# Kernel optimization log

Measured on AMD Instinct MI355X. Metric: run time of the kernel, lower is better.

The kernel has to match this reference:

```python
import jax, jax.numpy as jnp
import numpy as np

H = 4          # num_heads
K_HOP = 2
EPS = 1e-5


def _ln(x, g, b):
    m = jnp.mean(x, axis=-1, keepdims=True)
    v = jnp.mean((x - m) ** 2, axis=-1, keepdims=True)
    return (x - m) * jax.lax.rsqrt(v + EPS) * g + b


def setup_inputs() -> dict:
    key = jax.random.key(0)
    B, T, N, D = 16, 24, 512, 64
    F = 256
    ks = jax.random.split(key, 16)
    s = 0.02
    inp = {
        'x': jax.random.normal(ks[0], (B, T, N, D), dtype=jnp.float32),
        'adj': jax.random.uniform(ks[1], (N, N), dtype=jnp.float32),
        'Wq': jax.random.normal(ks[2], (D, D), dtype=jnp.float32) * s,
        'bq': jnp.zeros((D,), jnp.float32),
        'Wk': jax.random.normal(ks[3], (D, D), dtype=jnp.float32) * s,
        'bk': jnp.zeros((D,), jnp.float32),
        'Wv': jax.random.normal(ks[4], (D, D), dtype=jnp.float32) * s,
        'bv': jnp.zeros((D,), jnp.float32),
        'Wo': jax.random.normal(ks[5], (D, D), dtype=jnp.float32) * s,
        'bo': jnp.zeros((D,), jnp.float32),
        'gcW': jax.random.normal(ks[6], (K_HOP + 1, D, D), dtype=jnp.float32) * s,
        'gcb': jnp.zeros((K_HOP + 1, D), jnp.float32),
        'W1': jax.random.normal(ks[7], (D, F), dtype=jnp.float32) * s,
        'b1': jnp.zeros((F,), jnp.float32),
        'W2': jax.random.normal(ks[8], (F, D), dtype=jnp.float32) * s,
        'b2': jnp.zeros((D,), jnp.float32),
        'g_t': jnp.ones((D,), jnp.float32), 'b_t': jnp.zeros((D,), jnp.float32),
        'g_g': jnp.ones((D,), jnp.float32), 'b_g': jnp.zeros((D,), jnp.float32),
        'g_f': jnp.ones((D,), jnp.float32), 'b_f': jnp.zeros((D,), jnp.float32),
    }
    return inp


def _forward(x, adj, Wq, bq, Wk, bk, Wv, bv, Wo, bo, gcW, gcb,
             W1, b1, W2, b2, g_t, b_t, g_g, b_g, g_f, b_f):
    B, T, N, D = x.shape
    hd = D // H
    scale = hd ** -0.5

    # ---- temporal multi-head attention (per node, along T) ----
    def heads(y):
        return y.reshape(B, T, N, H, hd)
    q = heads(x @ Wq + bq)
    k = heads(x @ Wk + bk)
    v = heads(x @ Wv + bv)
    scores = jnp.einsum('bqnhd,bknhd->bnhqk', q, k) * scale  # [B,N,H,T,T]
    attn = jax.nn.softmax(scores, axis=-1)
    att = jnp.einsum('bnhqk,bknhd->bqnhd', attn, v).reshape(B, T, N, D)
    att = att @ Wo + bo
    h = _ln(x + att, g_t, b_t)

    # ---- K-hop graph convolution: sum_k A_hat^k X W_k ----
    A = adj + jnp.eye(N, dtype=adj.dtype)
    deg = A.sum(-1)
    dinv = jnp.clip(deg, 1e-12, None) ** -0.5
    Ahat = dinv[:, None] * A * dinv[None, :]  # [N,N], shared across B*T
    prop = h
    gout = prop @ gcW[0] + gcb[0]
    for kk in range(1, K_HOP + 1):
        prop = jnp.einsum('mn,btnd->btmd', Ahat, prop)
        gout = gout + prop @ gcW[kk] + gcb[kk]
    h = _ln(h + gout, g_g, b_g)

    # ---- FFN (exact GELU, as torch default) ----
    f = jax.nn.gelu(h @ W1 + b1, approximate=False) @ W2 + b2
    return _ln(h + f, g_f, b_f)


def reference(x, adj, Wq, bq, Wk, bk, Wv, bv, Wo, bo, gcW, gcb,
              W1, b1, W2, b2, g_t, b_t, g_g, b_g, g_f, b_f):
    return _forward(x, adj, Wq, bq, Wk, bk, Wv, bv, Wo, bo, gcW, gcb,
                    W1, b1, W2, b2, g_t, b_t, g_g, b_g, g_f, b_f)
```

## Files before the change

### kernel.cpp

```cpp
#include <hip/hip_runtime.h>
#include <hip/hip_bf16.h>
#include <math.h>

typedef __hip_bfloat16 bf16;
typedef unsigned short ushort_t;

__device__ __forceinline__ float us2f(ushort_t u){
  union { unsigned u; float f; } v; v.u = ((unsigned)u) << 16; return v.f;
}
__device__ __forceinline__ ushort_t f2us(float f){
  union { __bf16 b; ushort_t u; } v; v.b = (__bf16)f; return v.u;
}

__device__ __forceinline__ float gelu_f(float x){
  float y = x * fmaf(0.0356774081f, x*x, 0.7978845608f);
  float e = __expf(-2.0f*y);
  return x * __builtin_amdgcn_rcpf(1.0f + e);
}

#define B_ 16
#define T_ 24
#define N_ 512
#define D_ 64
#define F_ 256

typedef __attribute__((ext_vector_type(8)))  short  frag8;
typedef __attribute__((ext_vector_type(16))) float  accv16;

__device__ __forceinline__ float wave_sum(float v){
#pragma unroll
  for (int off = 32; off > 0; off >>= 1) v += __shfl_xor(v, off, 64);
  return v;
}

__global__ __launch_bounds__(64) void k_dinv(const float* __restrict__ adj,
                                             float* __restrict__ dinv){
  int m = blockIdx.x;
  float s = 0.f;
  for (int n = threadIdx.x; n < N_; n += 64) s += adj[m*N_ + n];
  s = wave_sum(s);
  if (threadIdx.x == 0){
    float deg = s + 1.0f;
    dinv[m] = rsqrtf(fmaxf(deg, 1e-12f));
  }
}

__global__ __launch_bounds__(256) void k_ahat(const float* __restrict__ adj,
                                              const float* __restrict__ dinv,
                                              ushort_t* __restrict__ AhatB,
                                              ushort_t* __restrict__ AhatBT){
  int idx = blockIdx.x*256 + threadIdx.x;
  int m = idx >> 9, n = idx & (N_-1);
  float a = adj[idx] + (m == n ? 1.f : 0.f);
  ushort_t v = f2us(dinv[m]*a*dinv[n]);
  AhatB[idx] = v;
  AhatBT[n*N_ + m] = v;
}

__global__ __launch_bounds__(256, 4) void k_ah2(
    const ushort_t* __restrict__ A1,
    const ushort_t* __restrict__ A1T,
    ushort_t* __restrict__ A2)
{
  __shared__ __align__(16) ushort_t Ab[64][72];
  __shared__ __align__(16) ushort_t Bb[64][72];
  __shared__ __align__(16) ushort_t Yt[64][72];
  int tid  = threadIdx.x;
  int lane = tid & 63, w = tid >> 6;
  int mw = (w >> 1) * 32, nw = (w & 1) * 32;
  int l31 = lane & 31, lh = lane >> 5;
  int m0 = blockIdx.x * 64, n0 = blockIdx.y * 64;
  int ar = tid >> 3, ac8 = (tid & 7) * 8;

  accv16 acc = {};
  for (int k0 = 0; k0 < N_; k0 += 64){
#pragma unroll
    for (int g = 0; g < 2; g++){
      int rr = ar + g*32;
      *(uint4*)&Ab[rr][ac8] = *(const uint4*)&A1 [(size_t)(m0 + rr)*N_ + k0 + ac8];
      *(uint4*)&Bb[rr][ac8] = *(const uint4*)&A1T[(size_t)(n0 + rr)*N_ + k0 + ac8];
    }
    __syncthreads();
#pragma unroll
    for (int kk = 0; kk < 64; kk += 16){
      frag8 af = *(const frag8*)&Ab[mw + l31][kk + lh*8];
      frag8 bf = *(const frag8*)&Bb[nw + l31][kk + lh*8];
      acc = __builtin_amdgcn_mfma_f32_32x32x16_bf16(af, bf, acc, 0, 0, 0);
    }
    __syncthreads();
  }
#pragma unroll
  for (int r = 0; r < 16; r++){
    int row = mw + (r & 3) + 8*(r >> 2) + 4*lh;
    Yt[row][nw + l31] = f2us(acc[r]);
  }
  __syncthreads();
#pragma unroll
  for (int g = 0; g < 2; g++){
    int rr = ar + g*32;
    *(uint4*)&A2[(size_t)(m0 + rr)*N_ + n0 + ac8] = *(const uint4*)&Yt[rr][ac8];
  }
}

__global__ __launch_bounds__(256) void k_wprep(
    const float* __restrict__ W1, const float* __restrict__ W2,
    const float* __restrict__ Wq, const float* __restrict__ Wk,
    const float* __restrict__ Wv, const float* __restrict__ Wo,
    const float* __restrict__ gcW,
    ushort_t* __restrict__ W1t, ushort_t* __restrict__ W2t,
    ushort_t* __restrict__ Wqt, ushort_t* __restrict__ Wkt,
    ushort_t* __restrict__ Wvt, ushort_t* __restrict__ Wot,
    ushort_t* __restrict__ gWt){
  int o = blockIdx.x*256 + threadIdx.x;
  int f = o >> 6, e = o & 63;
  W1t[o] = f2us(W1[e*256 + f]);
  int d = o >> 8, e2 = o & 255;
  W2t[o] = f2us(W2[e2*64 + d]);
  if (o < 4096){
    int dd = o >> 6, ee = o & 63;
    Wqt[o] = f2us(Wq[ee*64 + dd]);
    Wkt[o] = f2us(Wk[ee*64 + dd]);
    Wvt[o] = f2us(Wv[ee*64 + dd]);
    Wot[o] = f2us(Wo[ee*64 + dd]);
    gWt[o]        = f2us(gcW[       ee*64 + dd]);
    gWt[4096 + o] = f2us(gcW[4096 + ee*64 + dd]);
    gWt[8192 + o] = f2us(gcW[8192 + ee*64 + dd]);
  }
}

__global__ __launch_bounds__(256, 4) void k_attn_m(
    const float* __restrict__ x,
    const ushort_t* __restrict__ Wqt, const float* __restrict__ bq,
    const ushort_t* __restrict__ Wkt, const float* __restrict__ bk,
    const ushort_t* __restrict__ Wvt, const float* __restrict__ bv,
    const ushort_t* __restrict__ Wot, const float* __restrict__ bo,
    const float* __restrict__ g_t, const float* __restrict__ b_t,
    float* __restrict__ h1)
{
  __shared__ __align__(16) char smem[28928];
  ushort_t (*xsA)[72] = (ushort_t(*)[72]) smem;
  ushort_t (*qs)[72]  = (ushort_t(*)[72])(smem + 6912);
  ushort_t (*ks)[72]  = (ushort_t(*)[72])(smem + 13824);
  float    (*Os)[68]  = (float(*)[68])   (smem + 6912);
  ushort_t *vsT       = (ushort_t*)(smem + 20736);

  int tid = threadIdx.x;
  int lane = tid & 63, w = tid >> 6;
  int l31 = lane & 31, lh = lane >> 5;
  int mt = (w >> 1) * 32, nt = (w & 1) * 32;
  int b = blockIdx.x >> 8;
  int n0 = (blockIdx.x & 255) * 2;

  {
    uint4 z4 = {0,0,0,0};
#pragma unroll
    for (int i = 0; i < 2; i++)
      *(uint4*)(smem + 20736 + (tid + i*256)*16) = z4;
  }
#pragma unroll
  for (int i = 0; i < 3; i++){
    int idx = tid + i*256;
    int row = idx >> 4, d4 = (idx & 15) * 4;
    int node = row >= 24;
    int t = row - node*24;
    const float4 v = *(const float4*)&x[(((size_t)b*T_ + t)*N_ + n0 + node)*D_ + d4];
    ushort_t tmp[4] = { f2us(v.x), f2us(v.y), f2us(v.z), f2us(v.w) };
    *(unsigned long long*)&xsA[row][d4] = *(unsigned long long*)tmp;
  }
  __syncthreads();

#pragma unroll
  for (int pj = 0; pj < 3; pj++){
    const ushort_t* Wp = (pj==0 ? Wqt : pj==1 ? Wkt : Wvt);
    accv16 a = {};
#pragma unroll
    for (int kk = 0; kk < 64; kk += 16){
      frag8 af = *(const frag8*)&xsA[mt + l31][kk + lh*8];
      frag8 bf = *(const frag8*)&Wp[(size_t)(nt + l31)*64 + kk + lh*8];
      a = __builtin_amdgcn_mfma_f32_32x32x16_bf16(af, bf, a, 0, 0, 0);
    }
    float bias = (pj==0 ? bq : pj==1 ? bk : bv)[nt + l31];
    if (pj < 2){
      ushort_t (*dst)[72] = (pj==0 ? qs : ks);
#pragma unroll
      for (int r = 0; r < 16; r++){
        int row = mt + (r & 3) + 8*(r >> 2) + 4*lh;
        if (row < 48) dst[row][nt + l31] = f2us(a[r] + bias);
      }
    } else {
      int cl = nt + l31;
#pragma unroll
      for (int r = 0; r < 16; r++){
        int row = mt + (r & 3) + 8*(r >> 2) + 4*lh;
        if (row < 48){
          int node = (row >= 24);
          int t2 = row - node*24;
          int Rr = node*64 + cl;
          vsT[Rr*32 + (((t2 >> 3) ^ ((Rr >> 1) & 3)) << 3) + (t2 & 7)] = f2us(a[r] + bias);
        }
      }
    }
  }
  __syncthreads();

  int vs_s = (l31 >> 1) & 3;
#pragma unroll
  for (int gi = 0; gi < 2; gi++){
    int g = w*2 + gi;
    int node = g >> 2, hh = g & 3;
    accv16 s = {};
    frag8 kf = *(const frag8*)&ks[node*24 + l31][hh*16 + lh*8];
    frag8 qf = *(const frag8*)&qs[node*24 + l31][hh*16 + lh*8];
    s = __builtin_amdgcn_mfma_f32_32x32x16_bf16(kf, qf, s, 0, 0, 0);
    float e[12]; float sm = 0.f;
#pragma unroll
    for (int r = 0; r < 12; r++){ e[r] = __expf(s[r]*0.25f); sm += e[r]; }
    sm += __shfl_xor(sm, 32, 64);
    float rinv = 1.0f / sm;
    union { unsigned long long q; ushort_t u[4]; } a0, a1, a2;
#pragma unroll
    for (int j = 0; j < 4; j++){
      a0.u[j] = f2us(e[j]   * rinv);
      a1.u[j] = f2us(e[4+j] * rinv);
      a2.u[j] = f2us(e[8+j] * rinv);
    }
    unsigned long long send1 = lh ? a0.q : a1.q;
    unsigned long long r1 = __shfl_xor(send1, 32, 64);
    unsigned long long r2 = __shfl_xor(a2.q, 32, 64);
    union { frag8 f; unsigned long long q[2]; } f0, f1;
    f0.q[0] = lh ? r1   : a0.q;
    f0.q[1] = lh ? a1.q : r1;
    f1.q[0] = lh ? 0ULL : a2.q;
    f1.q[1] = lh ? 0ULL : r2;
    int vrow = node*64 + hh*16 + (l31 & 15);
    const ushort_t* vb = &vsT[vrow*32];
    frag8 bf0 = *(const frag8*)&vb[((0 + lh) ^ vs_s) << 3];
    frag8 bf1 = *(const frag8*)&vb[((2 + lh) ^ vs_s) << 3];
    accv16 acc = {};
    acc = __builtin_amdgcn_mfma_f32_32x32x16_bf16(f0.f, bf0, acc, 0, 0, 0);
    acc = __builtin_amdgcn_mfma_f32_32x32x16_bf16(f1.f, bf1, acc, 0, 0, 0);
    if (l31 < 16){
#pragma unroll
      for (int r = 0; r < 12; r++){
        int row = (r & 3) + 8*(r >> 2) + 4*lh;
        xsA[node*24 + row][hh*16 + l31] = f2us(acc[r]);
      }
    }
  }
  __syncthreads();

  accv16 ao = {};
#pragma unroll
  for (int kk = 0; kk < 64; kk += 16){
    frag8 af = *(const frag8*)&xsA[mt + l31][kk + lh*8];
    frag8 bf = *(const frag8*)&Wot[(size_t)(nt + l31)*64 + kk + lh*8];
    ao = __builtin_amdgcn_mfma_f32_32x32x16_bf16(af, bf, ao, 0, 0, 0);
  }
  {
    float bov = bo[nt + l31];
#pragma unroll
    for (int r = 0; r < 16; r++){
      int row = mt + (r & 3) + 8*(r >> 2) + 4*lh;
      if (row < 48) Os[row][nt + l31] = ao[r] + bov;
    }
  }
  __syncthreads();

  {
    int rrow = tid >> 2, seg = (tid & 3) * 16;
    if (rrow < 48){
      int node = rrow >= 24;
      int t = rrow - node*24;
      size_t gbase = (((size_t)b*T_ + t)*N_ + n0 + node)*D_;
      float vb[16]; float s1 = 0.f;
#pragma unroll
      for (int j4 = 0; j4 < 4; j4++){
        float4 xo = *(const float4*)&x[gbase + seg + j4*4];
        float4 ov = *(const float4*)&Os[rrow][seg + j4*4];
        vb[j4*4+0] = ov.x + xo.x;
        vb[j4*4+1] = ov.y + xo.y;
        vb[j4*4+2] = ov.z + xo.z;
        vb[j4*4+3] = ov.w + xo.w;
        s1 += vb[j4*4+0] + vb[j4*4+1] + vb[j4*4+2] + vb[j4*4+3];
      }
      s1 += __shfl_xor(s1, 1, 64); s1 += __shfl_xor(s1, 2, 64);
      float m = s1 * (1.f/64.f);
      float s2 = 0.f;
#pragma unroll
      for (int j = 0; j < 16; j++){ vb[j] -= m; s2 += vb[j]*vb[j]; }
      s2 += __shfl_xor(s2, 1, 64); s2 += __shfl_xor(s2, 2, 64);
      float rstd = rsqrtf(s2 * (1.f/64.f) + 1e-5f);
#pragma unroll
      for (int j4 = 0; j4 < 4; j4++){
        float4 gv = *(const float4*)&g_t[seg + j4*4];
        float4 bv = *(const float4*)&b_t[seg + j4*4];
        float4 st;
        st.x = vb[j4*4+0]*rstd*gv.x + bv.x;
        st.y = vb[j4*4+1]*rstd*gv.y + bv.y;
        st.z = vb[j4*4+2]*rstd*gv.z + bv.z;
        st.w = vb[j4*4+3]*rstd*gv.w + bv.w;
        *(float4*)&h1[gbase + seg + j4*4] = st;
      }
    }
  }
}

__global__ __launch_bounds__(256, 8) void k_hT(const float* __restrict__ h,
                                               ushort_t* __restrict__ hT){
  __shared__ __align__(16) ushort_t tb[64][76];
  int tid = threadIdx.x;
  int n0 = (blockIdx.x & 7) * 64;
  size_t bt = blockIdx.x >> 3;
  const float* src = h + (bt*N_ + n0)*D_;
#pragma unroll
  for (int i = 0; i < 4; i++){
    int q = tid + i*256;
    int row = q >> 4, d4 = (q & 15)*4;
    float4 v = *(const float4*)&src[(size_t)q*4];
    ushort_t tmp[4] = { f2us(v.x), f2us(v.y), f2us(v.z), f2us(v.w) };
    *(unsigned long long*)&tb[row][d4] = *(unsigned long long*)tmp;
  }
  __syncthreads();
  int d = tid >> 2, nseg = (tid & 3)*16;
  ushort_t tmp[16];
#pragma unroll
  for (int j = 0; j < 16; j++){
    int jj = (j + ((d & 7) << 1)) & 15;
    tmp[jj] = tb[nseg + jj][d];
  }
  ushort_t* dst = hT + (bt*D_ + d)*N_ + n0 + nseg;
  *(uint4*)&dst[0] = *(uint4*)&tmp[0];
  *(uint4*)&dst[8] = *(uint4*)&tmp[8];
}

__global__ __launch_bounds__(256, 4) void k_gcffn(
    const ushort_t* __restrict__ A1,
    const ushort_t* __restrict__ A2,
    const ushort_t* __restrict__ XT,
    const ushort_t* __restrict__ gWt,
    const float* __restrict__ gcb,
    const float* __restrict__ g_g, const float* __restrict__ b_g,
    const ushort_t* __restrict__ W1t, const ushort_t* __restrict__ W2t,
    const float* __restrict__ b1, const float* __restrict__ b2,
    const float* __restrict__ g_f, const float* __restrict__ b_f,
    float* __restrict__ h)
{
  __shared__ __align__(16) char smem[27648];
  ushort_t (*R0)[72]  = (ushort_t(*)[72]) smem;
  ushort_t (*R1)[72]  = (ushort_t(*)[72])(smem +  9216);
  ushort_t (*hsA)[72] = (ushort_t(*)[72])(smem + 18432);
  float    (*Sf)[68]  = (float(*)[68])    smem;
  ushort_t (*Uc)[136] = (ushort_t(*)[136])smem;
  float    (*Os)[68]  = (float(*)[68])    smem;

  int tid = threadIdx.x;
  int lane = tid & 63, w = tid >> 6;
  int l31 = lane & 31, lh = lane >> 5;
  int mw = (w >> 1) * 32, nw = (w & 1) * 32;
  int bid = blockIdx.x;
  int m0 = ((bid >> 3) & 7) * 64;
  size_t bt = (size_t)((bid >> 6) * 8 + (bid & 7));
  const ushort_t* Xg = XT + bt * (N_ * D_);
  size_t tokbase = bt * N_ + m0;
  int ar = tid >> 3, ac8 = (tid & 7) * 8;

  accv16 acc1 = {}, acc2 = {};
  for (int k0 = 0; k0 < N_; k0 += 64){
#pragma unroll
    for (int g = 0; g < 2; g++){
      int rr = ar + g*32;
      *(uint4*)&R0 [rr][ac8] = *(const uint4*)&A1[(size_t)(m0 + rr)*N_ + k0 + ac8];
      *(uint4*)&R1 [rr][ac8] = *(const uint4*)&A2[(size_t)(m0 + rr)*N_ + k0 + ac8];
      *(uint4*)&hsA[rr][ac8] = *(const uint4*)&Xg[(size_t)rr*N_ + k0 + ac8];
    }
    __syncthreads();
#pragma unroll
    for (int kk = 0; kk < 64; kk += 16){
      frag8 bf  = *(const frag8*)&hsA[nw + l31][kk + lh*8];
      frag8 af1 = *(const frag8*)&R0 [mw + l31][kk + lh*8];
      frag8 af2 = *(const frag8*)&R1 [mw + l31][kk + lh*8];
      acc1 = __builtin_amdgcn_mfma_f32_32x32x16_bf16(af1, bf, acc1, 0, 0, 0);
      acc2 = __builtin_amdgcn_mfma_f32_32x32x16_bf16(af2, bf, acc2, 0, 0, 0);
    }
    __syncthreads();
  }

#pragma unroll
  for (int r = 0; r < 16; r++){
    int row = mw + (r & 3) + 8*(r >> 2) + 4*lh;
    R1[row][nw + l31] = f2us(acc1[r]);
    R0[row][nw + l31] = f2us(acc2[r]);
  }
#pragma unroll
  for (int i = 0; i < 4; i++){
    int q = tid + i*256;
    int row = q >> 4, d4 = (q & 15) * 4;
    float4 v = *(const float4*)&h[tokbase*64 + (size_t)q*4];
    ushort_t tmp[4] = { f2us(v.x), f2us(v.y), f2us(v.z), f2us(v.w) };
    *(unsigned long long*)&hsA[row][d4] = *(unsigned long long*)tmp;
  }
  __syncthreads();

  accv16 ag = {};
#pragma unroll
  for (int kk = 0; kk < 64; kk += 16){
    frag8 a0f = *(const frag8*)&hsA[mw + l31][kk + lh*8];
    frag8 b0f = *(const frag8*)&gWt[(size_t)(nw + l31)*64 + kk + lh*8];
    ag = __builtin_amdgcn_mfma_f32_32x32x16_bf16(a0f, b0f, ag, 0, 0, 0);
  }
#pragma unroll
  for (int kk = 0; kk < 64; kk += 16){
    frag8 a1f = *(const frag8*)&R1[mw + l31][kk + lh*8];
    frag8 b1f = *(const frag8*)&gWt[4096 + (size_t)(nw + l31)*64 + kk + lh*8];
    ag = __builtin_amdgcn_mfma_f32_32x32x16_bf16(a1f, b1f, ag, 0, 0, 0);
  }
#pragma unroll
  for (int kk = 0; kk < 64; kk += 16){
    frag8 a2f = *(const frag8*)&R0[mw + l31][kk + lh*8];
    frag8 b2f = *(const frag8*)&gWt[8192 + (size_t)(nw + l31)*64 + kk + lh*8];
    ag = __builtin_amdgcn_mfma_f32_32x32x16_bf16(a2f, b2f, ag, 0, 0, 0);
  }
  __syncthreads();

  {
    int col = nw + l31;
    float bs = gcb[col] + gcb[64 + col] + gcb[128 + col];
#pragma unroll
    for (int r = 0; r < 16; r++){
      int row = mw + (r & 3) + 8*(r >> 2) + 4*lh;
      Sf[row][col] = ag[r] + h[(tokbase + row)*64 + col] + bs;
    }
  }
  __syncthreads();

  int rrow = tid >> 2, seg = (tid & 3) * 16;
  float h2r[16];
  {
    float vb[16]; float s1 = 0.f;
#pragma unroll
    for (int j4 = 0; j4 < 4; j4++){
      float4 v = *(const float4*)&Sf[rrow][seg + j4*4];
      vb[j4*4+0] = v.x; vb[j4*4+1] = v.y; vb[j4*4+2] = v.z; vb[j4*4+3] = v.w;
      s1 += v.x + v.y + v.z + v.w;
    }
    s1 += __shfl_xor(s1, 1, 64); s1 += __shfl_xor(s1, 2, 64);
    float m = s1 * (1.f/64.f);
    float s2 = 0.f;
#pragma unroll
    for (int j = 0; j < 16; j++){ vb[j] -= m; s2 += vb[j]*vb[j]; }
    s2 += __shfl_xor(s2, 1, 64); s2 += __shfl_xor(s2, 2, 64);
    float rstd = rsqrtf(s2 * (1.f/64.f) + 1e-5f);
    ushort_t tmp[16];
#pragma unroll
    for (int j4 = 0; j4 < 4; j4++){
      float4 gv = *(const float4*)&g_g[seg + j4*4];
      float4 bv = *(const float4*)&b_g[seg + j4*4];
      h2r[j4*4+0] = vb[j4*4+0]*rstd*gv.x + bv.x;
      h2r[j4*4+1] = vb[j4*4+1]*rstd*gv.y + bv.y;
      h2r[j4*4+2] = vb[j4*4+2]*rstd*gv.z + bv.z;
      h2r[j4*4+3] = vb[j4*4+3]*rstd*gv.w + bv.w;
    }
#pragma unroll
    for (int j = 0; j < 16; j++) tmp[j] = f2us(h2r[j]);
    *(uint4*)&hsA[rrow][seg]     = *(uint4*)&tmp[0];
    *(uint4*)&hsA[rrow][seg + 8] = *(uint4*)&tmp[8];
  }
  __syncthreads();

  int mw1 = (w & 1) * 32, nA = (w >> 1) * 32;
  int mw2 = (w >> 1) * 32, dw = (w & 1) * 32;
  accv16 accO = {};
#pragma unroll
  for (int f0 = 0; f0 < F_; f0 += 128){
    if (f0) __syncthreads();
    accv16 accA = {}, accB = {};
#pragma unroll
    for (int kk = 0; kk < 64; kk += 16){
      frag8 af  = *(const frag8*)&hsA[mw1 + l31][kk + lh*8];
      frag8 b0  = *(const frag8*)&W1t[(size_t)(f0 + nA + l31)*64 + kk + lh*8];
      frag8 b1f = *(const frag8*)&W1t[(size_t)(f0 + nA + 64 + l31)*64 + kk + lh*8];
      accA = __builtin_amdgcn_mfma_f32_32x32x16_bf16(af, b0,  accA, 0, 0, 0);
      accB = __builtin_amdgcn_mfma_f32_32x32x16_bf16(af, b1f, accB, 0, 0, 0);
    }
    {
      float bA = b1[f0 + nA + l31];
      float bB = b1[f0 + nA + 64 + l31];
#pragma unroll
      for (int r = 0; r < 16; r++){
        int row = mw1 + (r & 3) + 8*(r >> 2) + 4*lh;
        Uc[row][nA + l31]      = f2us(gelu_f(accA[r] + bA));
        Uc[row][nA + 64 + l31] = f2us(gelu_f(accB[r] + bB));
      }
    }
    __syncthreads();
#pragma unroll
    for (int kk = 0; kk < 128; kk += 16){
      frag8 af = *(const frag8*)&Uc[mw2 + l31][kk + lh*8];
      frag8 bf = *(const frag8*)&W2t[(size_t)(dw + l31)*256 + f0 + kk + lh*8];
      accO = __builtin_amdgcn_mfma_f32_32x32x16_bf16(af, bf, accO, 0, 0, 0);
    }
  }
  __syncthreads();
  {
    float b2v = b2[dw + l31];
#pragma unroll
    for (int r = 0; r < 16; r++){
      int row = mw2 + (r & 3) + 8*(r >> 2) + 4*lh;
      Os[row][dw + l31] = accO[r] + b2v;
    }
  }
  __syncthreads();

  {
    float vb[16]; float s1 = 0.f;
#pragma unroll
    for (int j4 = 0; j4 < 4; j4++){
      float4 v = *(const float4*)&Os[rrow][seg + j4*4];
      vb[j4*4+0] = v.x + h2r[j4*4+0];
      vb[j4*4+1] = v.y + h2r[j4*4+1];
      vb[j4*4+2] = v.z + h2r[j4*4+2];
      vb[j4*4+3] = v.w + h2r[j4*4+3];
      s1 += vb[j4*4+0] + vb[j4*4+1] + vb[j4*4+2] + vb[j4*4+3];
    }
    s1 += __shfl_xor(s1, 1, 64); s1 += __shfl_xor(s1, 2, 64);
    float m = s1 * (1.f/64.f);
    float s2 = 0.f;
#pragma unroll
    for (int j = 0; j < 16; j++){ vb[j] -= m; s2 += vb[j]*vb[j]; }
    s2 += __shfl_xor(s2, 1, 64); s2 += __shfl_xor(s2, 2, 64);
    float rstd = rsqrtf(s2 * (1.f/64.f) + 1e-5f);
#pragma unroll
    for (int j4 = 0; j4 < 4; j4++){
      float4 gv = *(const float4*)&g_f[seg + j4*4];
      float4 bv = *(const float4*)&b_f[seg + j4*4];
      float4 st;
      st.x = vb[j4*4+0]*rstd*gv.x + bv.x;
      st.y = vb[j4*4+1]*rstd*gv.y + bv.y;
      st.z = vb[j4*4+2]*rstd*gv.z + bv.z;
      st.w = vb[j4*4+3]*rstd*gv.w + bv.w;
      *(float4*)&h[(tokbase + rrow)*64 + seg + j4*4] = st;
    }
  }
}

extern "C" void kernel_launch(void* const* d_in, const int* in_sizes, int n_in,
                              void* d_out, int out_size, void* d_ws, size_t ws_size,
                              hipStream_t stream)
{
  const float* x   = (const float*)d_in[0];
  const float* adj = (const float*)d_in[1];
  const float* Wq  = (const float*)d_in[2];
  const float* bq  = (const float*)d_in[3];
  const float* Wk  = (const float*)d_in[4];
  const float* bk  = (const float*)d_in[5];
  const float* Wv  = (const float*)d_in[6];
  const float* bv  = (const float*)d_in[7];
  const float* Wo  = (const float*)d_in[8];
  const float* bo  = (const float*)d_in[9];
  const float* gcW = (const float*)d_in[10];
  const float* gcb = (const float*)d_in[11];
  const float* W1  = (const float*)d_in[12];
  const float* b1  = (const float*)d_in[13];
  const float* W2  = (const float*)d_in[14];
  const float* b2  = (const float*)d_in[15];
  const float* g_t = (const float*)d_in[16];
  const float* b_t = (const float*)d_in[17];
  const float* g_g = (const float*)d_in[18];
  const float* b_g = (const float*)d_in[19];
  const float* g_f = (const float*)d_in[20];
  const float* b_f = (const float*)d_in[21];

  const size_t MD = (size_t)B_*T_*N_*D_;
  const size_t NN = (size_t)N_*N_;
  float* dinv = (float*)d_ws;
  ushort_t* AhatB  = (ushort_t*)(dinv + 512);
  ushort_t* AhatBT = AhatB + NN;
  ushort_t* AhatB2 = AhatBT + NN;
  ushort_t* hT  = AhatB2 + NN;
  ushort_t* W1t = hT + MD;
  ushort_t* W2t = W1t + 256*64;
  ushort_t* Wqt = W2t + 64*256;
  ushort_t* Wkt = Wqt + 4096;
  ushort_t* Wvt = Wkt + 4096;
  ushort_t* Wot = Wvt + 4096;
  ushort_t* gWt = Wot + 4096;
  float* h = (float*)d_out;

  k_dinv<<<N_, 64, 0, stream>>>(adj, dinv);
  k_ahat<<<(N_*N_)/256, 256, 0, stream>>>(adj, dinv, AhatB, AhatBT);
  k_wprep<<<64, 256, 0, stream>>>(W1, W2, Wq, Wk, Wv, Wo, gcW,
                                  W1t, W2t, Wqt, Wkt, Wvt, Wot, gWt);
  k_ah2<<<dim3(8, 8), 256, 0, stream>>>(AhatB, AhatBT, AhatB2);
  k_attn_m<<<B_*N_/2, 256, 0, stream>>>(x, Wqt,bq, Wkt,bk, Wvt,bv, Wot,bo, g_t,b_t, h);
  k_hT<<<B_*T_*8, 256, 0, stream>>>(h, hT);
  k_gcffn<<<(N_/64) * B_ * T_, 256, 0, stream>>>(AhatB, AhatB2, hT, gWt,
                                                 gcb, g_g, b_g,
                                                 W1t, W2t, b1, b2, g_f, b_f, h);
}
```

Before: 340.8 us.

## Process two bt slices per block in graph-conv kernel to reuse Ahat tiles

Each k_gcffn block now handles two (b,t) slices sharing the same 64-row Ahat/Ahat² tiles, so each A tile loaded into shared memory feeds four MFMA accumulators instead of two. The grid is halved and shared memory grows to 36 KB. The epilogue (graph-conv weight GEMMs, layernorm, FFN) runs sequentially for each slice. The change cuts global and L2 traffic for Ahat, at the cost of more registers (four accumulators plus two h2r arrays), which may lower occupancy under the launch_bounds(256,4) hint.

```diff
diff --git a/kernel.cpp b/kernel.cpp
--- a/kernel.cpp
+++ b/kernel.cpp
@@ -345,10 +345,11 @@
     const float* __restrict__ g_f, const float* __restrict__ b_f,
     float* __restrict__ h)
 {
-  __shared__ __align__(16) char smem[27648];
-  ushort_t (*R0)[72]  = (ushort_t(*)[72]) smem;
-  ushort_t (*R1)[72]  = (ushort_t(*)[72])(smem +  9216);
-  ushort_t (*hsA)[72] = (ushort_t(*)[72])(smem + 18432);
+  __shared__ __align__(16) char smem[36864];
+  ushort_t (*RA1)[72] = (ushort_t(*)[72]) smem;
+  ushort_t (*RA2)[72] = (ushort_t(*)[72])(smem +  9216);
+  ushort_t (*RX0)[72] = (ushort_t(*)[72])(smem + 18432);
+  ushort_t (*RX1)[72] = (ushort_t(*)[72])(smem + 27648);
   float    (*Sf)[68]  = (float(*)[68])    smem;
   ushort_t (*Uc)[136] = (ushort_t(*)[136])smem;
   float    (*Os)[68]  = (float(*)[68])    smem;
@@ -358,189 +359,244 @@
   int l31 = lane & 31, lh = lane >> 5;
   int mw = (w >> 1) * 32, nw = (w & 1) * 32;
   int bid = blockIdx.x;
+  int xq = bid & 7;
   int m0 = ((bid >> 3) & 7) * 64;
-  size_t bt = (size_t)((bid >> 6) * 8 + (bid & 7));
-  const ushort_t* Xg = XT + bt * (N_ * D_);
-  size_t tokbase = bt * N_ + m0;
+  int q  = bid >> 6;
+  size_t bt0 = (size_t)(q*16 + xq);
+  size_t bt1 = bt0 + 8;
+  const ushort_t* Xg0 = XT + bt0 * (N_ * D_);
+  const ushort_t* Xg1 = XT + bt1 * (N_ * D_);
+  size_t tokb0 = bt0 * N_ + m0;
+  size_t tokb1 = bt1 * N_ + m0;
   int ar = tid >> 3, ac8 = (tid & 7) * 8;
 
-  accv16 acc1 = {}, acc2 = {};
+  accv16 a1s0 = {}, a2s0 = {}, a1s1 = {}, a2s1 = {};
   for (int k0 = 0; k0 < N_; k0 += 64){
 #pragma unroll
     for (int g = 0; g < 2; g++){
       int rr = ar + g*32;
-      *(uint4*)&R0 [rr][ac8] = *(const uint4*)&A1[(size_t)(m0 + rr)*N_ + k0 + ac8];
-      *(uint4*)&R1 [rr][ac8] = *(const uint4*)&A2[(size_t)(m0 + rr)*N_ + k0 + ac8];
-      *(uint4*)&hsA[rr][ac8] = *(const uint4*)&Xg[(size_t)rr*N_ + k0 + ac8];
-    }
-    __syncthreads();
-#pragma unroll
-    for (int kk = 0; kk < 64; kk += 16){
-      frag8 bf  = *(const frag8*)&hsA[nw + l31][kk + lh*8];
-      frag8 af1 = *(const frag8*)&R0 [mw + l31][kk + lh*8];
-      frag8 af2 = *(const frag8*)&R1 [mw + l31][kk + lh*8];
-      acc1 = __builtin_amdgcn_mfma_f32_32x32x16_bf16(af1, bf, acc1, 0, 0, 0);
-      acc2 = __builtin_amdgcn_mfma_f32_32x32x16_bf16(af2, bf, acc2, 0, 0, 0);
-    }
-    __syncthreads();
-  }
-
-#pragma unroll
-  for (int r = 0; r < 16; r++){
-    int row = mw + (r & 3) + 8*(r >> 2) + 4*lh;
-    R1[row][nw + l31] = f2us(acc1[r]);
-    R0[row][nw + l31] = f2us(acc2[r]);
-  }
-#pragma unroll
-  for (int i = 0; i < 4; i++){
-    int q = tid + i*256;
-    int row = q >> 4, d4 = (q & 15) * 4;
-    float4 v = *(const float4*)&h[tokbase*64 + (size_t)q*4];
-    ushort_t tmp[4] = { f2us(v.x), f2us(v.y), f2us(v.z), f2us(v.w) };
-    *(unsigned long long*)&hsA[row][d4] = *(unsigned long long*)tmp;
-  }
-  __syncthreads();
-
-  accv16 ag = {};
-#pragma unroll
-  for (int kk = 0; kk < 64; kk += 16){
-    frag8 a0f = *(const frag8*)&hsA[mw + l31][kk + lh*8];
-    frag8 b0f = *(const frag8*)&gWt[(size_t)(nw + l31)*64 + kk + lh*8];
-    ag = __builtin_amdgcn_mfma_f32_32x32x16_bf16(a0f, b0f, ag, 0, 0, 0);
-  }
-#pragma unroll
-  for (int kk = 0; kk < 64; kk += 16){
-    frag8 a1f = *(const frag8*)&R1[mw + l31][kk + lh*8];
-    frag8 b1f = *(const frag8*)&gWt[4096 + (size_t)(nw + l31)*64 + kk + lh*8];
-    ag = __builtin_amdgcn_mfma_f32_32x32x16_bf16(a1f, b1f, ag, 0, 0, 0);
-  }
-#pragma unroll
-  for (int kk = 0; kk < 64; kk += 16){
-    frag8 a2f = *(const frag8*)&R0[mw + l31][kk + lh*8];
-    frag8 b2f = *(const frag8*)&gWt[8192 + (size_t)(nw + l31)*64 + kk + lh*8];
-    ag = __builtin_amdgcn_mfma_f32_32x32x16_bf16(a2f, b2f, ag, 0, 0, 0);
-  }
-  __syncthreads();
-
+      *(uint4*)&RA1[rr][ac8] = *(const uint4*)&A1 [(size_t)(m0 + rr)*N_ + k0 + ac8];
+      *(uint4*)&RA2[rr][ac8] = *(const uint4*)&A2 [(size_t)(m0 + rr)*N_ + k0 + ac8];
+      *(uint4*)&RX0[rr][ac8] = *(const uint4*)&Xg0[(size_t)rr*N_ + k0 + ac8];
+      *(uint4*)&RX1[rr][ac8] = *(const uint4*)&Xg1[(size_t)rr*N_ + k0 + ac8];
+    }
+    __syncthreads();
+#pragma unroll
+    for (int kk = 0; kk < 64; kk += 16){
+      frag8 bf0 = *(const frag8*)&RX0[nw + l31][kk + lh*8];
+      frag8 bf1 = *(const frag8*)&RX1[nw + l31][kk + lh*8];
+      frag8 af1 = *(const frag8*)&RA1[mw + l31][kk + lh*8];
+      frag8 af2 = *(const frag8*)&RA2[mw + l31][kk + lh*8];
+      a1s0 = __builtin_amdgcn_mfma_f32_32x32x16_bf16(af1, bf0, a1s0, 0, 0, 0);
+      a2s0 = __builtin_amdgcn_mfma_f32_32x32x16_bf16(af2, bf0, a2s0, 0, 0, 0);
+      a1s1 = __builtin_amdgcn_mfma_f32_32x32x16_bf16(af1, bf1, a1s1, 0, 0, 0);
+      a2s1 = __builtin_amdgcn_mfma_f32_32x32x16_bf16(af2, bf1, a2s1, 0, 0, 0);
+    }
+    __syncthreads();
+  }
+
+  accv16 ag0 = {}, ag1 = {};
+  {
+#pragma unroll
+    for (int r = 0; r < 16; r++){
+      int row = mw + (r & 3) + 8*(r >> 2) + 4*lh;
+      RA1[row][nw + l31] = f2us(a1s0[r]);
+      RA2[row][nw + l31] = f2us(a2s0[r]);
+    }
+#pragma unroll
+    for (int i = 0; i < 4; i++){
+      int qq = tid + i*256;
+      int row = qq >> 4, d4 = (qq & 15) * 4;
+      float4 v = *(const float4*)&h[tokb0*64 + (size_t)qq*4];
+      ushort_t tmp[4] = { f2us(v.x), f2us(v.y), f2us(v.z), f2us(v.w) };
+      *(unsigned long long*)&RX0[row][d4] = *(unsigned long long*)tmp;
+    }
+    __syncthreads();
+#pragma unroll
+    for (int kk = 0; kk < 64; kk += 16){
+      frag8 a0f = *(const frag8*)&RX0[mw + l31][kk + lh*8];
+      frag8 b0f = *(const frag8*)&gWt[(size_t)(nw + l31)*64 + kk + lh*8];
+      ag0 = __builtin_amdgcn_mfma_f32_32x32x16_bf16(a0f, b0f, ag0, 0, 0, 0);
+    }
+#pragma unroll
+    for (int kk = 0; kk < 64; kk += 16){
+      frag8 a1f = *(const frag8*)&RA1[mw + l31][kk + lh*8];
+      frag8 b1f = *(const frag8*)&gWt[4096 + (size_t)(nw + l31)*64 + kk + lh*8];
+      ag0 = __builtin_amdgcn_mfma_f32_32x32x16_bf16(a1f, b1f, ag0, 0, 0, 0);
+    }
+#pragma unroll
+    for (int kk = 0; kk < 64; kk += 16){
+      frag8 a2f = *(const frag8*)&RA2[mw + l31][kk + lh*8];
+      frag8 b2f = *(const frag8*)&gWt[8192 + (size_t)(nw + l31)*64 + kk + lh*8];
+      ag0 = __builtin_amdgcn_mfma_f32_32x32x16_bf16(a2f, b2f, ag0, 0, 0, 0);
+    }
+    __syncthreads();
+  }
+  {
+#pragma unroll
+    for (int r = 0; r < 16; r++){
+      int row = mw + (r & 3) + 8*(r >> 2) + 4*lh;
+      RA1[row][nw + l31] = f2us(a1s1[r]);
+      RA2[row][nw + l31] = f2us(a2s1[r]);
+    }
+#pragma unroll
+    for (int i = 0; i < 4; i++){
+      int qq = tid + i*256;
+      int row = qq >> 4, d4 = (qq & 15) * 4;
+      float4 v = *(const float4*)&h[tokb1*64 + (size_t)qq*4];
+      ushort_t tmp[4] = { f2us(v.x), f2us(v.y), f2us(v.z), f2us(v.w) };
+      *(unsigned long long*)&RX1[row][d4] = *(unsigned long long*)tmp;
+    }
+    __syncthreads();
+#pragma unroll
+    for (int kk = 0; kk < 64; kk += 16){
+      frag8 a0f = *(const frag8*)&RX1[mw + l31][kk + lh*8];
+      frag8 b0f = *(const frag8*)&gWt[(size_t)(nw + l31)*64 + kk + lh*8];
+      ag1 = __builtin_amdgcn_mfma_f32_32x32x16_bf16(a0f, b0f, ag1, 0, 0, 0);
+    }
+#pragma unroll
+    for (int kk = 0; kk < 64; kk += 16){
+      frag8 a1f = *(const frag8*)&RA1[mw + l31][kk + lh*8];
+      frag8 b1f = *(const frag8*)&gWt[4096 + (size_t)(nw + l31)*64 + kk + lh*8];
+      ag1 = __builtin_amdgcn_mfma_f32_32x32x16_bf16(a1f, b1f, ag1, 0, 0, 0);
+    }
+#pragma unroll
+    for (int kk = 0; kk < 64; kk += 16){
+      frag8 a2f = *(const frag8*)&RA2[mw + l31][kk + lh*8];
+      frag8 b2f = *(const frag8*)&gWt[8192 + (size_t)(nw + l31)*64 + kk + lh*8];
+      ag1 = __builtin_amdgcn_mfma_f32_32x32x16_bf16(a2f, b2f, ag1, 0, 0, 0);
+    }
+    __syncthreads();
+  }
+
+  int rrow = tid >> 2, seg = (tid & 3) * 16;
+  int mw1 = (w & 1) * 32, nA = (w >> 1) * 32;
+  int mw2 = (w >> 1) * 32, dw = (w & 1) * 32;
+  float bs_col;
   {
     int col = nw + l31;
-    float bs = gcb[col] + gcb[64 + col] + gcb[128 + col];
-#pragma unroll
-    for (int r = 0; r < 16; r++){
-      int row = mw + (r & 3) + 8*(r >> 2) + 4*lh;
-      Sf[row][col] = ag[r] + h[(tokbase + row)*64 + col] + bs;
-    }
-  }
-  __syncthreads();
-
-  int rrow = tid >> 2, seg = (tid & 3) * 16;
-  float h2r[16];
-  {
-    float vb[16]; float s1 = 0.f;
-#pragma unroll
-    for (int j4 = 0; j4 < 4; j4++){
-      float4 v = *(const float4*)&Sf[rrow][seg + j4*4];
-      vb[j4*4+0] = v.x; vb[j4*4+1] = v.y; vb[j4*4+2] = v.z; vb[j4*4+3] = v.w;
-      s1 += v.x + v.y + v.z + v.w;
-    }
-    s1 += __shfl_xor(s1, 1, 64); s1 += __shfl_xor(s1, 2, 64);
-    float m = s1 * (1.f/64.f);
-    float s2 = 0.f;
-#pragma unroll
-    for (int j = 0; j < 16; j++){ vb[j] -= m; s2 += vb[j]*vb[j]; }
-    s2 += __shfl_xor(s2, 1, 64); s2 += __shfl_xor(s2, 2, 64);
-    float rstd = rsqrtf(s2 * (1.f/64.f) + 1e-5f);
-    ushort_t tmp[16];
-#pragma unroll
-    for (int j4 = 0; j4 < 4; j4++){
-      float4 gv = *(const float4*)&g_g[seg + j4*4];
-      float4 bv = *(const float4*)&b_g[seg + j4*4];
-      h2r[j4*4+0] = vb[j4*4+0]*rstd*gv.x + bv.x;
-      h2r[j4*4+1] = vb[j4*4+1]*rstd*gv.y + bv.y;
-      h2r[j4*4+2] = vb[j4*4+2]*rstd*gv.z + bv.z;
-      h2r[j4*4+3] = vb[j4*4+3]*rstd*gv.w + bv.w;
-    }
-#pragma unroll
-    for (int j = 0; j < 16; j++) tmp[j] = f2us(h2r[j]);
-    *(uint4*)&hsA[rrow][seg]     = *(uint4*)&tmp[0];
-    *(uint4*)&hsA[rrow][seg + 8] = *(uint4*)&tmp[8];
-  }
-  __syncthreads();
-
-  int mw1 = (w & 1) * 32, nA = (w >> 1) * 32;
-  int mw2 = (w >> 1) * 32, dw = (w & 1) * 32;
-  accv16 accO = {};
-#pragma unroll
-  for (int f0 = 0; f0 < F_; f0 += 128){
-    if (f0) __syncthreads();
-    accv16 accA = {}, accB = {};
-#pragma unroll
-    for (int kk = 0; kk < 64; kk += 16){
-      frag8 af  = *(const frag8*)&hsA[mw1 + l31][kk + lh*8];
-      frag8 b0  = *(const frag8*)&W1t[(size_t)(f0 + nA + l31)*64 + kk + lh*8];
-      frag8 b1f = *(const frag8*)&W1t[(size_t)(f0 + nA + 64 + l31)*64 + kk + lh*8];
-      accA = __builtin_amdgcn_mfma_f32_32x32x16_bf16(af, b0,  accA, 0, 0, 0);
-      accB = __builtin_amdgcn_mfma_f32_32x32x16_bf16(af, b1f, accB, 0, 0, 0);
-    }
-    {
-      float bA = b1[f0 + nA + l31];
-      float bB = b1[f0 + nA + 64 + l31];
-#pragma unroll
-      for (int r = 0; r < 16; r++){
-        int row = mw1 + (r & 3) + 8*(r >> 2) + 4*lh;
-        Uc[row][nA + l31]      = f2us(gelu_f(accA[r] + bA));
-        Uc[row][nA + 64 + l31] = f2us(gelu_f(accB[r] + bB));
-      }
-    }
-    __syncthreads();
-#pragma unroll
-    for (int kk = 0; kk < 128; kk += 16){
-      frag8 af = *(const frag8*)&Uc[mw2 + l31][kk + lh*8];
-      frag8 bf = *(const frag8*)&W2t[(size_t)(dw + l31)*256 + f0 + kk + lh*8];
-      accO = __builtin_amdgcn_mfma_f32_32x32x16_bf16(af, bf, accO, 0, 0, 0);
-    }
-  }
-  __syncthreads();
-  {
-    float b2v = b2[dw + l31];
-#pragma unroll
-    for (int r = 0; r < 16; r++){
-      int row = mw2 + (r & 3) + 8*(r >> 2) + 4*lh;
-      Os[row][dw + l31] = accO[r] + b2v;
-    }
-  }
-  __syncthreads();
-
-  {
-    float vb[16]; float s1 = 0.f;
-#pragma unroll
-    for (int j4 = 0; j4 < 4; j4++){
-      float4 v = *(const float4*)&Os[rrow][seg + j4*4];
-      vb[j4*4+0] = v.x + h2r[j4*4+0];
-      vb[j4*4+1] = v.y + h2r[j4*4+1];
-      vb[j4*4+2] = v.z + h2r[j4*4+2];
-      vb[j4*4+3] = v.w + h2r[j4*4+3];
-      s1 += vb[j4*4+0] + vb[j4*4+1] + vb[j4*4+2] + vb[j4*4+3];
-    }
-    s1 += __shfl_xor(s1, 1, 64); s1 += __shfl_xor(s1, 2, 64);
-    float m = s1 * (1.f/64.f);
-    float s2 = 0.f;
-#pragma unroll
-    for (int j = 0; j < 16; j++){ vb[j] -= m; s2 += vb[j]*vb[j]; }
-    s2 += __shfl_xor(s2, 1, 64); s2 += __shfl_xor(s2, 2, 64);
-    float rstd = rsqrtf(s2 * (1.f/64.f) + 1e-5f);
-#pragma unroll
-    for (int j4 = 0; j4 < 4; j4++){
-      float4 gv = *(const float4*)&g_f[seg + j4*4];
-      float4 bv = *(const float4*)&b_f[seg + j4*4];
-      float4 st;
-      st.x = vb[j4*4+0]*rstd*gv.x + bv.x;
-      st.y = vb[j4*4+1]*rstd*gv.y + bv.y;
-      st.z = vb[j4*4+2]*rstd*gv.z + bv.z;
-      st.w = vb[j4*4+3]*rstd*gv.w + bv.w;
-      *(float4*)&h[(tokbase + rrow)*64 + seg + j4*4] = st;
-    }
-  }
+    bs_col = gcb[col] + gcb[64 + col] + gcb[128 + col];
+  }
+
+#define SLICE_EPI(AG, RXS, TOKB, H2R)                                         \
+  {                                                                           \
+    int col = nw + l31;                                                       \
+    _Pragma("unroll")                                                         \
+    for (int r = 0; r < 16; r++){                                             \
+      int row = mw + (r & 3) + 8*(r >> 2) + 4*lh;                             \
+      Sf[row][col] = AG[r] + h[(TOKB + row)*64 + col] + bs_col;               \
+    }                                                                         \
+    __syncthreads();                                                          \
+    {                                                                         \
+      float vb[16]; float s1 = 0.f;                                           \
+      _Pragma("unroll")                                                       \
+      for (int j4 = 0; j4 < 4; j4++){                                         \
+        float4 v = *(const float4*)&Sf[rrow][seg + j4*4];                     \
+        vb[j4*4+0] = v.x; vb[j4*4+1] = v.y;                                   \
+        vb[j4*4+2] = v.z; vb[j4*4+3] = v.w;                                   \
+        s1 += v.x + v.y + v.z + v.w;                                          \
+      }                                                                       \
+      s1 += __shfl_xor(s1, 1, 64); s1 += __shfl_xor(s1, 2, 64);               \
+      float m = s1 * (1.f/64.f);                                              \
+      float s2 = 0.f;                                                         \
+      _Pragma("unroll")                                                       \
+      for (int j = 0; j < 16; j++){ vb[j] -= m; s2 += vb[j]*vb[j]; }          \
+      s2 += __shfl_xor(s2, 1, 64); s2 += __shfl_xor(s2, 2, 64);               \
+      float rstd = rsqrtf(s2 * (1.f/64.f) + 1e-5f);                           \
+      ushort_t tmp[16];                                                       \
+      _Pragma("unroll")                                                       \
+      for (int j4 = 0; j4 < 4; j4++){                                         \
+        float4 gv = *(const float4*)&g_g[seg + j4*4];                         \
+        float4 bv = *(const float4*)&b_g[seg + j4*4];                         \
+        H2R[j4*4+0] = vb[j4*4+0]*rstd*gv.x + bv.x;                            \
+        H2R[j4*4+1] = vb[j4*4+1]*rstd*gv.y + bv.y;                            \
+        H2R[j4*4+2] = vb[j4*4+2]*rstd*gv.z + bv.z;                            \
+        H2R[j4*4+3] = vb[j4*4+3]*rstd*gv.w + bv.w;                            \
+      }                                                                       \
+      _Pragma("unroll")                                                       \
+      for (int j = 0; j < 16; j++) tmp[j] = f2us(H2R[j]);                     \
+      *(uint4*)&RXS[rrow][seg]     = *(uint4*)&tmp[0];                        \
+      *(uint4*)&RXS[rrow][seg + 8] = *(uint4*)&tmp[8];                        \
+    }                                                                         \
+    __syncthreads();                                                          \
+    accv16 accO = {};                                                         \
+    _Pragma("unroll")                                                         \
+    for (int f0 = 0; f0 < F_; f0 += 128){                                     \
+      if (f0) __syncthreads();                                                \
+      accv16 accA = {}, accB = {};                                            \
+      _Pragma("unroll")                                                       \
+      for (int kk = 0; kk < 64; kk += 16){                                    \
+        frag8 af  = *(const frag8*)&RXS[mw1 + l31][kk + lh*8];                \
+        frag8 b0  = *(const frag8*)&W1t[(size_t)(f0 + nA + l31)*64 + kk + lh*8]; \
+        frag8 b1f = *(const frag8*)&W1t[(size_t)(f0 + nA + 64 + l31)*64 + kk + lh*8]; \
+        accA = __builtin_amdgcn_mfma_f32_32x32x16_bf16(af, b0,  accA, 0, 0, 0); \
+        accB = __builtin_amdgcn_mfma_f32_32x32x16_bf16(af, b1f, accB, 0, 0, 0); \
+      }                                                                       \
+      {                                                                       \
+        float bA = b1[f0 + nA + l31];                                         \
+        float bB = b1[f0 + nA + 64 + l31];                                    \
+        _Pragma("unroll")                                                     \
+        for (int r = 0; r < 16; r++){                                         \
+          int row = mw1 + (r & 3) + 8*(r >> 2) + 4*lh;                        \
+          Uc[row][nA + l31]      = f2us(gelu_f(accA[r] + bA));                \
+          Uc[row][nA + 64 + l31] = f2us(gelu_f(accB[r] + bB));                \
+        }                                                                     \
+      }                                                                       \
+      __syncthreads();                                                        \
+      _Pragma("unroll")                                                       \
+      for (int kk = 0; kk < 128; kk += 16){                                   \
+        frag8 af = *(const frag8*)&Uc[mw2 + l31][kk + lh*8];                  \
+        frag8 bf = *(const frag8*)&W2t[(size_t)(dw + l31)*256 + f0 + kk + lh*8]; \
+        accO = __builtin_amdgcn_mfma_f32_32x32x16_bf16(af, bf, accO, 0, 0, 0);\
+      }                                                                       \
+    }                                                                         \
+    __syncthreads();                                                          \
+    {                                                                         \
+      float b2v = b2[dw + l31];                                               \
+      _Pragma("unroll")                                                       \
+      for (int r = 0; r < 16; r++){                                           \
+        int row = mw2 + (r & 3) + 8*(r >> 2) + 4*lh;                          \
+        Os[row][dw + l31] = accO[r] + b2v;                                    \
+      }                                                                       \
+    }                                                                         \
+    __syncthreads();                                                          \
+    {                                                                         \
+      float vb[16]; float s1 = 0.f;                                           \
+      _Pragma("unroll")                                                       \
+      for (int j4 = 0; j4 < 4; j4++){                                         \
+        float4 v = *(const float4*)&Os[rrow][seg + j4*4];                     \
+        vb[j4*4+0] = v.x + H2R[j4*4+0];                                       \
+        vb[j4*4+1] = v.y + H2R[j4*4+1];                                       \
+        vb[j4*4+2] = v.z + H2R[j4*4+2];                                       \
+        vb[j4*4+3] = v.w + H2R[j4*4+3];                                       \
+        s1 += vb[j4*4+0] + vb[j4*4+1] + vb[j4*4+2] + vb[j4*4+3];              \
+      }                                                                       \
+      s1 += __shfl_xor(s1, 1, 64); s1 += __shfl_xor(s1, 2, 64);               \
+      float m = s1 * (1.f/64.f);                                              \
+      float s2 = 0.f;                                                         \
+      _Pragma("unroll")                                                       \
+      for (int j = 0; j < 16; j++){ vb[j] -= m; s2 += vb[j]*vb[j]; }          \
+      s2 += __shfl_xor(s2, 1, 64); s2 += __shfl_xor(s2, 2, 64);               \
+      float rstd = rsqrtf(s2 * (1.f/64.f) + 1e-5f);                           \
+      _Pragma("unroll")                                                       \
+      for (int j4 = 0; j4 < 4; j4++){                                         \
+        float4 gv = *(const float4*)&g_f[seg + j4*4];                         \
+        float4 bv = *(const float4*)&b_f[seg + j4*4];                         \
+        float4 st;                                                            \
+        st.x = vb[j4*4+0]*rstd*gv.x + bv.x;                                   \
+        st.y = vb[j4*4+1]*rstd*gv.y + bv.y;                                   \
+        st.z = vb[j4*4+2]*rstd*gv.z + bv.z;                                   \
+        st.w = vb[j4*4+3]*rstd*gv.w + bv.w;                                   \
+        *(float4*)&h[(TOKB + rrow)*64 + seg + j4*4] = st;                     \
+      }                                                                       \
+    }                                                                         \
+    __syncthreads();                                                          \
+  }
+
+  float h2r0[16], h2r1[16];
+  SLICE_EPI(ag0, RX0, tokb0, h2r0)
+  SLICE_EPI(ag1, RX1, tokb1, h2r1)
+#undef SLICE_EPI
 }
 
 extern "C" void kernel_launch(void* const* d_in, const int* in_sizes, int n_in,
@@ -593,7 +649,7 @@
   k_ah2<<<dim3(8, 8), 256, 0, stream>>>(AhatB, AhatBT, AhatB2);
   k_attn_m<<<B_*N_/2, 256, 0, stream>>>(x, Wqt,bq, Wkt,bk, Wvt,bv, Wot,bo, g_t,b_t, h);
   k_hT<<<B_*T_*8, 256, 0, stream>>>(h, hT);
-  k_gcffn<<<(N_/64) * B_ * T_, 256, 0, stream>>>(AhatB, AhatB2, hT, gWt,
-                                                 gcb, g_g, b_g,
-                                                 W1t, W2t, b1, b2, g_f, b_f, h);
-}
+  k_gcffn<<<(N_/64) * B_ * T_ / 2, 256, 0, stream>>>(AhatB, AhatB2, hT, gWt,
+                                                     gcb, g_g, b_g,
+                                                     W1t, W2t, b1, b2, g_f, b_f, h);
+}
```

New measurement: 410.7 us. 1.21x slower.
